# Kernel optimization log

Measured on AMD Instinct MI355X. Metric: run time of the kernel, lower is better.

The kernel has to match this reference:

```python
import jax, jax.numpy as jnp
import numpy as np

B, S, DM = 4, 2048, 512
H, D = 8, 64          # att_head, head_dim = att_dim // att_head
LEFT, RIGHT = 128, 128  # band_part(left_mask, right_mask)
LARGE = 1e30          # masked_softmax large number for fp32


def setup_inputs() -> dict:
    key = jax.random.key(0)
    ks = jax.random.split(key, 11)
    scale = 1.0 / np.sqrt(DM)
    x = jax.random.normal(ks[0], (B, S, DM), jnp.float32)
    Wq = jax.random.normal(ks[1], (DM, DM), jnp.float32) * scale
    bq = jnp.zeros((DM,), jnp.float32)
    Wk = jax.random.normal(ks[2], (DM, DM), jnp.float32) * scale
    bk = jnp.zeros((DM,), jnp.float32)
    Wv = jax.random.normal(ks[3], (DM, DM), jnp.float32) * scale
    bv = jnp.zeros((DM,), jnp.float32)
    Wo = jax.random.normal(ks[4], (DM, DM), jnp.float32) * scale
    bo = jnp.zeros((DM,), jnp.float32)
    x_len = jax.random.randint(ks[5], (B,), 0, 2048)
    return {"x": x, "Wq": Wq, "bq": bq, "Wk": Wk, "bk": bk,
            "Wv": Wv, "bv": bv, "Wo": Wo, "bo": bo, "x_len": x_len}


def reference(x, Wq, bq, Wk, bk, Wv, bv, Wo, bo, x_len):
    b, s, _ = x.shape
    # QKV projections, split into heads: [B,S,H,D]
    q = (x @ Wq + bq).reshape(b, s, H, D)
    k = (x @ Wk + bk).reshape(b, s, H, D)
    v = (x @ Wv + bv).reshape(b, s, H, D)
    # content energy: [B,H,Q,K], scaled by sqrt(head_dim)
    energy = jnp.einsum('bind,bjnd->bnij', q, k) / jnp.sqrt(jnp.float32(D))
    # banded mask (tf.linalg.band_part semantics): keep -LEFT <= j-i <= RIGHT
    i = jnp.arange(s)[:, None]
    j = jnp.arange(s)[None, :]
    band = ((j - i) <= RIGHT) & ((i - j) <= LEFT)            # [S,S]
    # key-length mask (tf.sequence_mask, expanded to [B,1,1,S])
    seq = jnp.arange(s)[None, :] < x_len[:, None]            # [B,S]
    mask = (band[None, None, :, :] & seq[:, None, None, :]).astype(energy.dtype)
    # masked softmax: energy - (1 - mask) * LARGE, softmax over keys
    att = jax.nn.softmax(energy - (1.0 - mask) * LARGE, axis=-1)
    # context: [B,Q,H,D] -> [B,S,H*D]
    ctx = jnp.einsum('bnij,bjnd->bind', att, v).reshape(b, s, H * D)
    # output projection (use_proj=True)
    return ctx @ Wo + bo
```

## Files before the change

### kernel.cpp

```cpp
#include <hip/hip_runtime.h>

#define S_LEN 2048
#define BATCH 4
#define DMODEL 512
#define NHEAD 8
#define HDIM 64
#define ROWS (BATCH * S_LEN)

using short8 = __attribute__((ext_vector_type(8))) short;
using f32x4  = __attribute__((ext_vector_type(4))) float;

__device__ __forceinline__ unsigned short f2bf(float f) {
  unsigned int u = __builtin_bit_cast(unsigned int, f);
  u += 0x7fffu + ((u >> 16) & 1u);
  return (unsigned short)(u >> 16);
}
__device__ __forceinline__ float bf2f(unsigned short h) {
  unsigned int u = ((unsigned int)h) << 16;
  return __builtin_bit_cast(float, u);
}
__device__ __forceinline__ void glds16(const void* g, void* l) {
  __builtin_amdgcn_global_load_lds((const __attribute__((address_space(1))) unsigned*)g,
                                   (__attribute__((address_space(3))) unsigned*)l, 16, 0, 0);
}

__global__ __launch_bounds__(256) void prep_kernel(const float* __restrict__ x,
                                                   const float* __restrict__ Wq,
                                                   const float* __restrict__ Wk,
                                                   const float* __restrict__ Wv,
                                                   const float* __restrict__ Wo,
                                                   unsigned short* __restrict__ xb,
                                                   unsigned short* __restrict__ WqkT,
                                                   unsigned short* __restrict__ WvT,
                                                   unsigned short* __restrict__ WoT) {
  __shared__ float t[32][33];
  const int blk = blockIdx.x, tid = threadIdx.x;
  if (blk < 2048) {
    const int base = (blk * 256 + tid) * 8;
    float4 f0 = *(const float4*)(x + base);
    float4 f1 = *(const float4*)(x + base + 4);
    uint4 o;
    o.x = (unsigned)f2bf(f0.x) | ((unsigned)f2bf(f0.y) << 16);
    o.y = (unsigned)f2bf(f0.z) | ((unsigned)f2bf(f0.w) << 16);
    o.z = (unsigned)f2bf(f1.x) | ((unsigned)f2bf(f1.y) << 16);
    o.w = (unsigned)f2bf(f1.z) | ((unsigned)f2bf(f1.w) << 16);
    *(uint4*)(xb + base) = o;
    return;
  }
  const int tb = blk - 2048;
  const int which = tb >> 8;
  const int tile = tb & 255;
  const float* W = which == 0 ? Wq : which == 1 ? Wk : which == 2 ? Wv : Wo;
  unsigned short* WT = which == 0 ? WqkT : which == 1 ? (WqkT + 512 * 512)
                      : which == 2 ? WvT : WoT;
  const int tx = tid & 31, ty = tid >> 5;
  const int x0 = (tile & 15) * 32, y0 = (tile >> 4) * 32;
#pragma unroll
  for (int r = 0; r < 4; r++)
    t[ty + 8 * r][tx] = W[(size_t)(y0 + ty + 8 * r) * DMODEL + x0 + tx];
  __syncthreads();
#pragma unroll
  for (int r = 0; r < 4; r++)
    WT[(size_t)(x0 + ty + 8 * r) * DMODEL + y0 + tx] = f2bf(t[tx][ty + 8 * r]);
}

__global__ __launch_bounds__(256, 2) void gemm_qkv_kernel(const unsigned short* __restrict__ xb,
                                                          const unsigned short* __restrict__ WqkT,
                                                          const unsigned short* __restrict__ WvT,
                                                          const float* __restrict__ bq,
                                                          const float* __restrict__ bk,
                                                          const float* __restrict__ bv,
                                                          const int* __restrict__ x_len,
                                                          unsigned short* __restrict__ Qb,
                                                          unsigned short* __restrict__ Kb,
                                                          unsigned short* __restrict__ Vt) {
  constexpr int K = DMODEL;
  __shared__ __align__(16) char smem[16384];
  char* As = smem;
  char* Bs = smem + 8192;
  const int bid = blockIdx.x;
  const bool vmode = bid < 256;
  const unsigned short *A, *Bt;
  int m0, n0;
  if (vmode) {
    m0 = (bid & 3) * 128;
    n0 = (bid >> 2) * 128;
    A = WvT; Bt = xb;
  } else {
    const int q = bid - 256;
    m0 = (q >> 3) * 128;
    n0 = (q & 7) * 128;
    A = xb; Bt = WqkT;
    const int xl = x_len[m0 >> 11];
    const int s0 = m0 & 2047;
    if (n0 >= DMODEL) { if (s0 >= xl) return; }
    else if (s0 >= xl + 128) return;
  }
  const int tid = threadIdx.x;
  const int wave = tid >> 6, lane = tid & 63;
  const int wr = wave >> 1, wc = wave & 1;
  const int lm = lane & 15, lq = lane >> 4;
  const int lr = lane >> 2;
  const int lc = (lane & 3) ^ ((lane >> 3) & 3);
  const unsigned short* gA0 = A + (size_t)(m0 + wave * 16 + lr) * K + lc * 8;
  const unsigned short* gA1 = A + (size_t)(m0 + (wave + 4) * 16 + lr) * K + lc * 8;
  const unsigned short* gB0 = Bt + (size_t)(n0 + wave * 16 + lr) * K + lc * 8;
  const unsigned short* gB1 = Bt + (size_t)(n0 + (wave + 4) * 16 + lr) * K + lc * 8;
  char* lA0 = As + wave * 1024 + lane * 16;
  char* lA1 = As + (wave + 4) * 1024 + lane * 16;
  char* lB0 = Bs + wave * 1024 + lane * 16;
  char* lB1 = Bs + (wave + 4) * 1024 + lane * 16;
  const int sw = (lm >> 1) & 3;
  int aoff[4], boff[4];
#pragma unroll
  for (int mi = 0; mi < 4; mi++)
    aoff[mi] = (wr * 64 + mi * 16 + lm) * 64 + (lq ^ sw) * 16;
#pragma unroll
  for (int ni = 0; ni < 4; ni++)
    boff[ni] = (wc * 64 + ni * 16 + lm) * 64 + (lq ^ sw) * 16;

  f32x4 acc[4][4] = {};
  for (int k0 = 0; k0 < K; k0 += 32) {
    __syncthreads();
    glds16(gA0 + k0, lA0);
    glds16(gA1 + k0, lA1);
    glds16(gB0 + k0, lB0);
    glds16(gB1 + k0, lB1);
    __syncthreads();
    short8 af[4], bfr[4];
#pragma unroll
    for (int mi = 0; mi < 4; mi++) af[mi] = *(const short8*)(As + aoff[mi]);
#pragma unroll
    for (int ni = 0; ni < 4; ni++) bfr[ni] = *(const short8*)(Bs + boff[ni]);
#pragma unroll
    for (int mi = 0; mi < 4; mi++)
#pragma unroll
      for (int ni = 0; ni < 4; ni++)
        acc[mi][ni] = __builtin_amdgcn_mfma_f32_16x16x32_bf16(af[mi], bfr[ni], acc[mi][ni], 0, 0, 0);
  }
#pragma unroll
  for (int mi = 0; mi < 4; mi++) {
    const int row0 = m0 + wr * 64 + mi * 16 + lq * 4;
#pragma unroll
    for (int ni = 0; ni < 4; ni++) {
      const int col = n0 + wc * 64 + ni * 16 + lm;
#pragma unroll
      for (int r = 0; r < 4; r++) {
        const int row = row0 + r;
        const float v = acc[mi][ni][r];
        if (vmode) {
          Vt[(size_t)row * ROWS + col] = f2bf(v + bv[row]);
        } else if (col < DMODEL) {
          Qb[(size_t)row * DMODEL + col] = f2bf(v + bq[col]);
        } else {
          Kb[(size_t)row * DMODEL + (col - DMODEL)] = f2bf(v + bk[col - DMODEL]);
        }
      }
    }
  }
}

__global__ __launch_bounds__(256, 2) void gemm_out_kernel(const unsigned short* __restrict__ A,
                                                          const unsigned short* __restrict__ Bt,
                                                          const float* __restrict__ bias,
                                                          float* __restrict__ out) {
  constexpr int K = DMODEL;
  __shared__ __align__(16) char smem[16384];
  char* As = smem;
  char* Bs = smem + 8192;
  const int tid = threadIdx.x;
  const int wave = tid >> 6, lane = tid & 63;
  const int wr = wave >> 1, wc = wave & 1;
  const int lm = lane & 15, lq = lane >> 4;
  const int m0 = blockIdx.y * 128, n0 = blockIdx.x * 128;
  const int lr = lane >> 2;
  const int lc = (lane & 3) ^ ((lane >> 3) & 3);
  const unsigned short* gA0 = A + (size_t)(m0 + wave * 16 + lr) * K + lc * 8;
  const unsigned short* gA1 = A + (size_t)(m0 + (wave + 4) * 16 + lr) * K + lc * 8;
  const unsigned short* gB0 = Bt + (size_t)(n0 + wave * 16 + lr) * K + lc * 8;
  const unsigned short* gB1 = Bt + (size_t)(n0 + (wave + 4) * 16 + lr) * K + lc * 8;
  char* lA0 = As + wave * 1024 + lane * 16;
  char* lA1 = As + (wave + 4) * 1024 + lane * 16;
  char* lB0 = Bs + wave * 1024 + lane * 16;
  char* lB1 = Bs + (wave + 4) * 1024 + lane * 16;
  const int sw = (lm >> 1) & 3;
  int aoff[4], boff[4];
#pragma unroll
  for (int mi = 0; mi < 4; mi++)
    aoff[mi] = (wr * 64 + mi * 16 + lm) * 64 + (lq ^ sw) * 16;
#pragma unroll
  for (int ni = 0; ni < 4; ni++)
    boff[ni] = (wc * 64 + ni * 16 + lm) * 64 + (lq ^ sw) * 16;

  f32x4 acc[4][4] = {};
  for (int k0 = 0; k0 < K; k0 += 32) {
    __syncthreads();
    glds16(gA0 + k0, lA0);
    glds16(gA1 + k0, lA1);
    glds16(gB0 + k0, lB0);
    glds16(gB1 + k0, lB1);
    __syncthreads();
    short8 af[4], bfr[4];
#pragma unroll
    for (int mi = 0; mi < 4; mi++) af[mi] = *(const short8*)(As + aoff[mi]);
#pragma unroll
    for (int ni = 0; ni < 4; ni++) bfr[ni] = *(const short8*)(Bs + boff[ni]);
#pragma unroll
    for (int mi = 0; mi < 4; mi++)
#pragma unroll
      for (int ni = 0; ni < 4; ni++)
        acc[mi][ni] = __builtin_amdgcn_mfma_f32_16x16x32_bf16(af[mi], bfr[ni], acc[mi][ni], 0, 0, 0);
  }
#pragma unroll
  for (int mi = 0; mi < 4; mi++) {
    const int row0 = m0 + wr * 64 + mi * 16 + lq * 4;
#pragma unroll
    for (int ni = 0; ni < 4; ni++) {
      const int col = n0 + wc * 64 + ni * 16 + lm;
#pragma unroll
      for (int r = 0; r < 4; r++)
        out[(size_t)(row0 + r) * DMODEL + col] = acc[mi][ni][r] + bias[col];
    }
  }
}

__global__ __launch_bounds__(256) void vsum_kernel(const unsigned short* __restrict__ Vt,
                                                   float* __restrict__ vs) {
  const int wid = blockIdx.x * 4 + (threadIdx.x >> 6);
  const int lane = threadIdx.x & 63;
  const int b = wid >> 9, n = wid & 511;
  const unsigned short* row = Vt + (size_t)n * ROWS + b * S_LEN;
  float s = 0.f;
#pragma unroll
  for (int it = 0; it < 4; it++) {
    uint4 v = *(const uint4*)(row + it * 512 + lane * 8);
    unsigned int w[4] = {v.x, v.y, v.z, v.w};
#pragma unroll
    for (int e = 0; e < 4; e++) {
      s += bf2f((unsigned short)(w[e] & 0xffffu));
      s += bf2f((unsigned short)(w[e] >> 16));
    }
  }
#pragma unroll
  for (int off = 1; off < 64; off <<= 1) s += __shfl_xor(s, off, 64);
  if (lane == 0) vs[(size_t)b * DMODEL + n] = s;
}

__global__ __launch_bounds__(256) void attn_kernel(const unsigned short* __restrict__ Q,
                                                   const unsigned short* __restrict__ K,
                                                   const unsigned short* __restrict__ Vt,
                                                   const int* __restrict__ x_len,
                                                   const float* __restrict__ vsum,
                                                   unsigned short* __restrict__ ctx) {
  __shared__ unsigned short Ks[32][72];
  __shared__ unsigned short Vs[64][40];
  __shared__ unsigned short Ps[4][16][40];
  const int tid = threadIdx.x;
  const int wave = tid >> 6, lane = tid & 63;
  const int lm = lane & 15, lq = lane >> 4;
  const int b = blockIdx.z, h = blockIdx.y;
  const int i0 = blockIdx.x * 64;
  const int q0 = i0 + wave * 16;
  const int xlen = x_len[b];

  const size_t qoff = (size_t)(b * S_LEN + q0 + lm) * DMODEL + h * HDIM + lq * 8;
  const short8 aq0 = *(const short8*)(Q + qoff);
  const short8 aq1 = *(const short8*)(Q + qoff + 32);

  const int krow = tid >> 3, kchk = (tid & 7) * 8;
  const int vdim = tid >> 2, vchk = (tid & 3) * 8;

  f32x4 oacc[4] = {};
  float lrow[4] = {0.f, 0.f, 0.f, 0.f};

  for (int kt = 0; kt < 10; kt++) {
    const int jt0 = i0 - 128 + kt * 32;
    if (jt0 + 31 < 0 || jt0 >= xlen) continue;
    __syncthreads();
    {
      const int jr = jt0 + krow;
      const int jrc = min(max(jr, 0), S_LEN - 1);
      *(uint4*)&Ks[krow][kchk] =
          *(const uint4*)(K + (size_t)(b * S_LEN + jrc) * DMODEL + h * HDIM + kchk);
      const int jv = jt0 + vchk;
      const int jvc = min(max(jv, 0), S_LEN - 8);
      *(uint4*)&Vs[vdim][vchk] =
          *(const uint4*)(Vt + (size_t)(h * HDIM + vdim) * ROWS + b * S_LEN + jvc);
    }
    __syncthreads();
    if (jt0 + 31 < q0 - 128 || jt0 > q0 + 143) continue;

    f32x4 sv[2];
#pragma unroll
    for (int sub = 0; sub < 2; sub++) {
      const short8 bk0 = *(const short8*)&Ks[sub * 16 + lm][lq * 8];
      const short8 bk1 = *(const short8*)&Ks[sub * 16 + lm][32 + lq * 8];
      f32x4 s = {};
      s = __builtin_amdgcn_mfma_f32_16x16x32_bf16(aq0, bk0, s, 0, 0, 0);
      s = __builtin_amdgcn_mfma_f32_16x16x32_bf16(aq1, bk1, s, 0, 0, 0);
      sv[sub] = s;
    }
    float p[2][4];
#pragma unroll
    for (int sub = 0; sub < 2; sub++) {
      const int j = jt0 + sub * 16 + lm;
      const bool jv = (j >= 0) && (j < xlen);
#pragma unroll
      for (int r = 0; r < 4; r++) {
        const int i = q0 + lq * 4 + r;
        const bool ok = jv && (j - i <= 128) && (i - j <= 128);
        const float pv = ok ? __expf(sv[sub][r] * 0.125f) : 0.f;
        p[sub][r] = pv;
        lrow[r] += pv;
      }
    }
#pragma unroll
    for (int r = 0; r < 4; r++) {
      Ps[wave][lq * 4 + r][lm] = f2bf(p[0][r]);
      Ps[wave][lq * 4 + r][16 + lm] = f2bf(p[1][r]);
    }
    const short8 pf = *(const short8*)&Ps[wave][lm][lq * 8];
#pragma unroll
    for (int dt = 0; dt < 4; dt++) {
      const short8 bv = *(const short8*)&Vs[dt * 16 + lm][lq * 8];
      oacc[dt] = __builtin_amdgcn_mfma_f32_16x16x32_bf16(pf, bv, oacc[dt], 0, 0, 0);
    }
  }
#pragma unroll
  for (int r = 0; r < 4; r++)
#pragma unroll
    for (int off = 1; off < 16; off <<= 1) lrow[r] += __shfl_xor(lrow[r], off, 64);

#pragma unroll
  for (int r = 0; r < 4; r++) {
    const int i = q0 + lq * 4 + r;
    const size_t obase = (size_t)(b * S_LEN + i) * DMODEL + h * HDIM;
    if (lrow[r] > 0.f) {
      const float inv = 1.f / lrow[r];
#pragma unroll
      for (int dt = 0; dt < 4; dt++)
        ctx[obase + dt * 16 + lm] = f2bf(oacc[dt][r] * inv);
    } else {
#pragma unroll
      for (int dt = 0; dt < 4; dt++)
        ctx[obase + dt * 16 + lm] =
            f2bf(vsum[(size_t)b * DMODEL + h * HDIM + dt * 16 + lm] * (1.f / 2048.f));
    }
  }
}

extern "C" void kernel_launch(void* const* d_in, const int* in_sizes, int n_in,
                              void* d_out, int out_size, void* d_ws, size_t ws_size,
                              hipStream_t stream) {
  (void)in_sizes; (void)n_in; (void)out_size; (void)ws_size;
  const float* x  = (const float*)d_in[0];
  const float* Wq = (const float*)d_in[1];
  const float* bq = (const float*)d_in[2];
  const float* Wk = (const float*)d_in[3];
  const float* bk = (const float*)d_in[4];
  const float* Wv = (const float*)d_in[5];
  const float* bv = (const float*)d_in[6];
  const float* Wo = (const float*)d_in[7];
  const float* bo = (const float*)d_in[8];
  const int* x_len = (const int*)d_in[9];

  char* ws = (char*)d_ws;
  const size_t MB = 1024 * 1024;
  unsigned short* xb   = (unsigned short*)(ws + 0 * MB);
  unsigned short* Qb   = (unsigned short*)(ws + 8 * MB);
  unsigned short* Kb   = (unsigned short*)(ws + 16 * MB);
  unsigned short* Vt   = (unsigned short*)(ws + 24 * MB);
  unsigned short* Cx   = (unsigned short*)(ws + 32 * MB);
  unsigned short* WqkT = (unsigned short*)(ws + 40 * MB);
  unsigned short* WvT  = (unsigned short*)(ws + 41 * MB);
  unsigned short* WoT  = (unsigned short*)(ws + 41 * MB + 512 * 1024);
  float* vsum          = (float*)(ws + 42 * MB);

  prep_kernel<<<3072, 256, 0, stream>>>(x, Wq, Wk, Wv, Wo, xb, WqkT, WvT, WoT);
  gemm_qkv_kernel<<<768, 256, 0, stream>>>(xb, WqkT, WvT, bq, bk, bv, x_len, Qb, Kb, Vt);
  vsum_kernel<<<512, 256, 0, stream>>>(Vt, vsum);
  attn_kernel<<<dim3(32, 8, 4), 256, 0, stream>>>(Qb, Kb, Vt, x_len, vsum, Cx);
  gemm_out_kernel<<<dim3(4, 64), 256, 0, stream>>>(Cx, WoT, bo, (float*)d_out);
}
```

Baseline: 149.3 us.

## Skip output GEMM for fully masked rows and use swizzled LDS loads in attention

Output-GEMM blocks whose rows all lie past x_len+128 now exit early. A new tail kernel writes those rows directly as the constant projection of the mean of V (vsum/2048 @ Wo + bo), which is what uniform softmax over fully masked rows gives. The attention kernel also switches its K/V tile loads to global_load_lds with an XOR-swizzled unpadded LDS layout, removing the register round-trip and padding. The tail kernel adds a naive per-block 512x512 matvec, which is redundant across blocks but small.

New measurement: 168.3 us. 12.7% more time.

```diff
diff --git a/kernel.cpp b/kernel.cpp
--- a/kernel.cpp
+++ b/kernel.cpp
@@ -163,16 +163,21 @@
 __global__ __launch_bounds__(256, 2) void gemm_out_kernel(const unsigned short* __restrict__ A,
                                                           const unsigned short* __restrict__ Bt,
                                                           const float* __restrict__ bias,
+                                                          const int* __restrict__ x_len,
                                                           float* __restrict__ out) {
   constexpr int K = DMODEL;
   __shared__ __align__(16) char smem[16384];
   char* As = smem;
   char* Bs = smem + 8192;
+  const int m0 = blockIdx.y * 128, n0 = blockIdx.x * 128;
+  {
+    const int xl = x_len[m0 >> 11];
+    if ((m0 & 2047) >= min(S_LEN, xl + 128)) return;
+  }
   const int tid = threadIdx.x;
   const int wave = tid >> 6, lane = tid & 63;
   const int wr = wave >> 1, wc = wave & 1;
   const int lm = lane & 15, lq = lane >> 4;
-  const int m0 = blockIdx.y * 128, n0 = blockIdx.x * 128;
   const int lr = lane >> 2;
   const int lc = (lane & 3) ^ ((lane >> 3) & 3);
   const unsigned short* gA0 = A + (size_t)(m0 + wave * 16 + lr) * K + lc * 8;
@@ -224,6 +229,30 @@
   }
 }
 
+__global__ __launch_bounds__(256) void tail_kernel(const float* __restrict__ vsum,
+                                                   const unsigned short* __restrict__ WoT,
+                                                   const float* __restrict__ bo,
+                                                   const int* __restrict__ x_len,
+                                                   float* __restrict__ out) {
+  const int b = blockIdx.y, j = blockIdx.x;
+  const int t0 = min(S_LEN, x_len[b] + 128);
+  const int r0 = j * 128, r1 = r0 + 128;
+  if (r1 <= t0) return;
+  __shared__ float tv[512];
+  const float* vs = vsum + b * DMODEL;
+  for (int c = threadIdx.x; c < DMODEL; c += 256) {
+    const unsigned short* wrow = WoT + (size_t)c * DMODEL;
+    float acc = 0.f;
+    for (int k = 0; k < DMODEL; k++) acc += vs[k] * bf2f(wrow[k]);
+    tv[c] = bo[c] + acc * (1.f / 2048.f);
+  }
+  __syncthreads();
+  const int rs = max(r0, t0);
+  const float4 val = ((const float4*)tv)[threadIdx.x & 127];
+  for (int r = rs + (threadIdx.x >> 7); r < r1; r += 2)
+    ((float4*)(out + (size_t)(b * S_LEN + r) * DMODEL))[threadIdx.x & 127] = val;
+}
+
 __global__ __launch_bounds__(256) void vsum_kernel(const unsigned short* __restrict__ Vt,
                                                    float* __restrict__ vs) {
   const int wid = blockIdx.x * 4 + (threadIdx.x >> 6);
@@ -252,8 +281,8 @@
                                                    const int* __restrict__ x_len,
                                                    const float* __restrict__ vsum,
                                                    unsigned short* __restrict__ ctx) {
-  __shared__ unsigned short Ks[32][72];
-  __shared__ unsigned short Vs[64][40];
+  __shared__ __align__(16) unsigned short Ks[32 * 64];
+  __shared__ __align__(16) unsigned short Vs[64 * 32];
   __shared__ unsigned short Ps[4][16][40];
   const int tid = threadIdx.x;
   const int wave = tid >> 6, lane = tid & 63;
@@ -267,8 +296,13 @@
   const short8 aq0 = *(const short8*)(Q + qoff);
   const short8 aq1 = *(const short8*)(Q + qoff + 32);
 
-  const int krow = tid >> 3, kchk = (tid & 7) * 8;
-  const int vdim = tid >> 2, vchk = (tid & 3) * 8;
+  const int kr = lane >> 3, kp = lane & 7, klc = kp ^ kr;
+  unsigned short* dstK = Ks + wave * 512 + lane * 8;
+  const int vr = lane >> 2, vp = lane & 3;
+  const int vrow = wave * 16 + vr;
+  const int vlc = vp ^ ((vr >> 1) & 3);
+  unsigned short* dstV = Vs + wave * 512 + lane * 8;
+  const int swk = lm & 7, swv = (lm >> 1) & 3;
 
   f32x4 oacc[4] = {};
   float lrow[4] = {0.f, 0.f, 0.f, 0.f};
@@ -278,14 +312,12 @@
     if (jt0 + 31 < 0 || jt0 >= xlen) continue;
     __syncthreads();
     {
-      const int jr = jt0 + krow;
-      const int jrc = min(max(jr, 0), S_LEN - 1);
-      *(uint4*)&Ks[krow][kchk] =
-          *(const uint4*)(K + (size_t)(b * S_LEN + jrc) * DMODEL + h * HDIM + kchk);
-      const int jv = jt0 + vchk;
+      const int krow_g = jt0 + wave * 8 + kr;
+      const int krc = min(max(krow_g, 0), S_LEN - 1);
+      glds16(K + (size_t)(b * S_LEN + krc) * DMODEL + h * HDIM + klc * 8, dstK);
+      const int jv = jt0 + vlc * 8;
       const int jvc = min(max(jv, 0), S_LEN - 8);
-      *(uint4*)&Vs[vdim][vchk] =
-          *(const uint4*)(Vt + (size_t)(h * HDIM + vdim) * ROWS + b * S_LEN + jvc);
+      glds16(Vt + (size_t)(h * HDIM + vrow) * ROWS + b * S_LEN + jvc, dstV);
     }
     __syncthreads();
     if (jt0 + 31 < q0 - 128 || jt0 > q0 + 143) continue;
@@ -293,8 +325,9 @@
     f32x4 sv[2];
 #pragma unroll
     for (int sub = 0; sub < 2; sub++) {
-      const short8 bk0 = *(const short8*)&Ks[sub * 16 + lm][lq * 8];
-      const short8 bk1 = *(const short8*)&Ks[sub * 16 + lm][32 + lq * 8];
+      const int krow = (sub * 16 + lm) * 64;
+      const short8 bk0 = *(const short8*)&Ks[krow + ((lq ^ swk) * 8)];
+      const short8 bk1 = *(const short8*)&Ks[krow + (((lq + 4) ^ swk) * 8)];
       f32x4 s = {};
       s = __builtin_amdgcn_mfma_f32_16x16x32_bf16(aq0, bk0, s, 0, 0, 0);
       s = __builtin_amdgcn_mfma_f32_16x16x32_bf16(aq1, bk1, s, 0, 0, 0);
@@ -322,7 +355,7 @@
     const short8 pf = *(const short8*)&Ps[wave][lm][lq * 8];
 #pragma unroll
     for (int dt = 0; dt < 4; dt++) {
-      const short8 bv = *(const short8*)&Vs[dt * 16 + lm][lq * 8];
+      const short8 bv = *(const short8*)&Vs[(dt * 16 + lm) * 32 + ((lq ^ swv) * 8)];
       oacc[dt] = __builtin_amdgcn_mfma_f32_16x16x32_bf16(pf, bv, oacc[dt], 0, 0, 0);
     }
   }
@@ -380,5 +413,6 @@
   gemm_qkv_kernel<<<768, 256, 0, stream>>>(xb, WqkT, WvT, bq, bk, bv, x_len, Qb, Kb, Vt);
   vsum_kernel<<<512, 256, 0, stream>>>(Vt, vsum);
   attn_kernel<<<dim3(32, 8, 4), 256, 0, stream>>>(Qb, Kb, Vt, x_len, vsum, Cx);
-  gemm_out_kernel<<<dim3(4, 64), 256, 0, stream>>>(Cx, WoT, bo, (float*)d_out);
-}
+  gemm_out_kernel<<<dim3(4, 64), 256, 0, stream>>>(Cx, WoT, bo, x_len, (float*)d_out);
+  tail_kernel<<<dim3(16, 4), 256, 0, stream>>>(vsum, WoT, bo, x_len, (float*)d_out);
+}
```

## Skip fully-masked query tiles; precompute shared output row for masked tail

Applied to the files above, without the earlier changes.

Query rows beyond x_len+128 have no valid keys, so their output is a constant row per batch: mean(V) projected through Wo plus bias. A small tailrow kernel computes this row once per batch. The attention kernel now exits early for those tiles, and the output GEMM fills those blocks by broadcasting the row instead of running the MFMA loop. This avoids attention and projection work on rows that are fully masked, at the cost of one extra small launch and a result that depends on the runtime x_len distribution.

Result: no change. 148.9 us (-0.2%).

```diff
diff --git a/kernel.cpp b/kernel.cpp
--- a/kernel.cpp
+++ b/kernel.cpp
@@ -160,70 +160,6 @@
   }
 }
 
-__global__ __launch_bounds__(256, 2) void gemm_out_kernel(const unsigned short* __restrict__ A,
-                                                          const unsigned short* __restrict__ Bt,
-                                                          const float* __restrict__ bias,
-                                                          float* __restrict__ out) {
-  constexpr int K = DMODEL;
-  __shared__ __align__(16) char smem[16384];
-  char* As = smem;
-  char* Bs = smem + 8192;
-  const int tid = threadIdx.x;
-  const int wave = tid >> 6, lane = tid & 63;
-  const int wr = wave >> 1, wc = wave & 1;
-  const int lm = lane & 15, lq = lane >> 4;
-  const int m0 = blockIdx.y * 128, n0 = blockIdx.x * 128;
-  const int lr = lane >> 2;
-  const int lc = (lane & 3) ^ ((lane >> 3) & 3);
-  const unsigned short* gA0 = A + (size_t)(m0 + wave * 16 + lr) * K + lc * 8;
-  const unsigned short* gA1 = A + (size_t)(m0 + (wave + 4) * 16 + lr) * K + lc * 8;
-  const unsigned short* gB0 = Bt + (size_t)(n0 + wave * 16 + lr) * K + lc * 8;
-  const unsigned short* gB1 = Bt + (size_t)(n0 + (wave + 4) * 16 + lr) * K + lc * 8;
-  char* lA0 = As + wave * 1024 + lane * 16;
-  char* lA1 = As + (wave + 4) * 1024 + lane * 16;
-  char* lB0 = Bs + wave * 1024 + lane * 16;
-  char* lB1 = Bs + (wave + 4) * 1024 + lane * 16;
-  const int sw = (lm >> 1) & 3;
-  int aoff[4], boff[4];
-#pragma unroll
-  for (int mi = 0; mi < 4; mi++)
-    aoff[mi] = (wr * 64 + mi * 16 + lm) * 64 + (lq ^ sw) * 16;
-#pragma unroll
-  for (int ni = 0; ni < 4; ni++)
-    boff[ni] = (wc * 64 + ni * 16 + lm) * 64 + (lq ^ sw) * 16;
-
-  f32x4 acc[4][4] = {};
-  for (int k0 = 0; k0 < K; k0 += 32) {
-    __syncthreads();
-    glds16(gA0 + k0, lA0);
-    glds16(gA1 + k0, lA1);
-    glds16(gB0 + k0, lB0);
-    glds16(gB1 + k0, lB1);
-    __syncthreads();
-    short8 af[4], bfr[4];
-#pragma unroll
-    for (int mi = 0; mi < 4; mi++) af[mi] = *(const short8*)(As + aoff[mi]);
-#pragma unroll
-    for (int ni = 0; ni < 4; ni++) bfr[ni] = *(const short8*)(Bs + boff[ni]);
-#pragma unroll
-    for (int mi = 0; mi < 4; mi++)
-#pragma unroll
-      for (int ni = 0; ni < 4; ni++)
-        acc[mi][ni] = __builtin_amdgcn_mfma_f32_16x16x32_bf16(af[mi], bfr[ni], acc[mi][ni], 0, 0, 0);
-  }
-#pragma unroll
-  for (int mi = 0; mi < 4; mi++) {
-    const int row0 = m0 + wr * 64 + mi * 16 + lq * 4;
-#pragma unroll
-    for (int ni = 0; ni < 4; ni++) {
-      const int col = n0 + wc * 64 + ni * 16 + lm;
-#pragma unroll
-      for (int r = 0; r < 4; r++)
-        out[(size_t)(row0 + r) * DMODEL + col] = acc[mi][ni][r] + bias[col];
-    }
-  }
-}
-
 __global__ __launch_bounds__(256) void vsum_kernel(const unsigned short* __restrict__ Vt,
                                                    float* __restrict__ vs) {
   const int wid = blockIdx.x * 4 + (threadIdx.x >> 6);
@@ -244,6 +180,33 @@
 #pragma unroll
   for (int off = 1; off < 64; off <<= 1) s += __shfl_xor(s, off, 64);
   if (lane == 0) vs[(size_t)b * DMODEL + n] = s;
+}
+
+__global__ __launch_bounds__(256) void tailrow_kernel(const float* __restrict__ vsum,
+                                                      const unsigned short* __restrict__ WoT,
+                                                      const float* __restrict__ bo,
+                                                      float* __restrict__ trow) {
+  const int b = blockIdx.y;
+  const int wave = threadIdx.x >> 6, lane = threadIdx.x & 63;
+  const float* vs = vsum + b * DMODEL + lane * 8;
+  float vreg[8];
+  *(float4*)vreg = *(const float4*)vs;
+  *(float4*)(vreg + 4) = *(const float4*)(vs + 4);
+#pragma unroll
+  for (int ci = 0; ci < 8; ci++) {
+    const int c = blockIdx.x * 32 + wave * 8 + ci;
+    const uint4 wv = *(const uint4*)(WoT + (size_t)c * DMODEL + lane * 8);
+    const unsigned int w[4] = {wv.x, wv.y, wv.z, wv.w};
+    float acc = 0.f;
+#pragma unroll
+    for (int e = 0; e < 4; e++) {
+      acc += vreg[2 * e] * bf2f((unsigned short)(w[e] & 0xffffu));
+      acc += vreg[2 * e + 1] * bf2f((unsigned short)(w[e] >> 16));
+    }
+#pragma unroll
+    for (int off = 1; off < 64; off <<= 1) acc += __shfl_xor(acc, off, 64);
+    if (lane == 0) trow[b * DMODEL + c] = bo[c] + acc * (1.f / 2048.f);
+  }
 }
 
 __global__ __launch_bounds__(256) void attn_kernel(const unsigned short* __restrict__ Q,
@@ -262,6 +225,8 @@
   const int i0 = blockIdx.x * 64;
   const int q0 = i0 + wave * 16;
   const int xlen = x_len[b];
+  const int t0 = min(S_LEN, xlen + 128);
+  if ((i0 & ~127) >= t0) return;
 
   const size_t qoff = (size_t)(b * S_LEN + q0 + lm) * DMODEL + h * HDIM + lq * 8;
   const short8 aq0 = *(const short8*)(Q + qoff);
@@ -345,6 +310,83 @@
       for (int dt = 0; dt < 4; dt++)
         ctx[obase + dt * 16 + lm] =
             f2bf(vsum[(size_t)b * DMODEL + h * HDIM + dt * 16 + lm] * (1.f / 2048.f));
+    }
+  }
+}
+
+__global__ __launch_bounds__(256, 2) void gemm_out_kernel(const unsigned short* __restrict__ A,
+                                                          const unsigned short* __restrict__ Bt,
+                                                          const float* __restrict__ bias,
+                                                          const int* __restrict__ x_len,
+                                                          const float* __restrict__ trow,
+                                                          float* __restrict__ out) {
+  constexpr int K = DMODEL;
+  __shared__ __align__(16) char smem[16384];
+  char* As = smem;
+  char* Bs = smem + 8192;
+  const int tid = threadIdx.x;
+  const int m0 = blockIdx.y * 128, n0 = blockIdx.x * 128;
+  {
+    const int xl = x_len[m0 >> 11];
+    if ((m0 & 2047) >= min(S_LEN, xl + 128)) {
+      const float4 val = *(const float4*)(trow + (m0 >> 11) * DMODEL + n0 + (tid & 31) * 4);
+      float* obase = out + (size_t)m0 * DMODEL + n0 + (tid & 31) * 4;
+#pragma unroll
+      for (int r = tid >> 5; r < 128; r += 8)
+        *(float4*)(obase + (size_t)r * DMODEL) = val;
+      return;
+    }
+  }
+  const int wave = tid >> 6, lane = tid & 63;
+  const int wr = wave >> 1, wc = wave & 1;
+  const int lm = lane & 15, lq = lane >> 4;
+  const int lr = lane >> 2;
+  const int lc = (lane & 3) ^ ((lane >> 3) & 3);
+  const unsigned short* gA0 = A + (size_t)(m0 + wave * 16 + lr) * K + lc * 8;
+  const unsigned short* gA1 = A + (size_t)(m0 + (wave + 4) * 16 + lr) * K + lc * 8;
+  const unsigned short* gB0 = Bt + (size_t)(n0 + wave * 16 + lr) * K + lc * 8;
+  const unsigned short* gB1 = Bt + (size_t)(n0 + (wave + 4) * 16 + lr) * K + lc * 8;
+  char* lA0 = As + wave * 1024 + lane * 16;
+  char* lA1 = As + (wave + 4) * 1024 + lane * 16;
+  char* lB0 = Bs + wave * 1024 + lane * 16;
+  char* lB1 = Bs + (wave + 4) * 1024 + lane * 16;
+  const int sw = (lm >> 1) & 3;
+  int aoff[4], boff[4];
+#pragma unroll
+  for (int mi = 0; mi < 4; mi++)
+    aoff[mi] = (wr * 64 + mi * 16 + lm) * 64 + (lq ^ sw) * 16;
+#pragma unroll
+  for (int ni = 0; ni < 4; ni++)
+    boff[ni] = (wc * 64 + ni * 16 + lm) * 64 + (lq ^ sw) * 16;
+
+  f32x4 acc[4][4] = {};
+  for (int k0 = 0; k0 < K; k0 += 32) {
+    __syncthreads();
+    glds16(gA0 + k0, lA0);
+    glds16(gA1 + k0, lA1);
+    glds16(gB0 + k0, lB0);
+    glds16(gB1 + k0, lB1);
+    __syncthreads();
+    short8 af[4], bfr[4];
+#pragma unroll
+    for (int mi = 0; mi < 4; mi++) af[mi] = *(const short8*)(As + aoff[mi]);
+#pragma unroll
+    for (int ni = 0; ni < 4; ni++) bfr[ni] = *(const short8*)(Bs + boff[ni]);
+#pragma unroll
+    for (int mi = 0; mi < 4; mi++)
+#pragma unroll
+      for (int ni = 0; ni < 4; ni++)
+        acc[mi][ni] = __builtin_amdgcn_mfma_f32_16x16x32_bf16(af[mi], bfr[ni], acc[mi][ni], 0, 0, 0);
+  }
+#pragma unroll
+  for (int mi = 0; mi < 4; mi++) {
+    const int row0 = m0 + wr * 64 + mi * 16 + lq * 4;
+#pragma unroll
+    for (int ni = 0; ni < 4; ni++) {
+      const int col = n0 + wc * 64 + ni * 16 + lm;
+#pragma unroll
+      for (int r = 0; r < 4; r++)
+        out[(size_t)(row0 + r) * DMODEL + col] = acc[mi][ni][r] + bias[col];
     }
   }
 }
@@ -375,10 +417,12 @@
   unsigned short* WvT  = (unsigned short*)(ws + 41 * MB);
   unsigned short* WoT  = (unsigned short*)(ws + 41 * MB + 512 * 1024);
   float* vsum          = (float*)(ws + 42 * MB);
+  float* trow          = (float*)(ws + 42 * MB + 8192);
 
   prep_kernel<<<3072, 256, 0, stream>>>(x, Wq, Wk, Wv, Wo, xb, WqkT, WvT, WoT);
   gemm_qkv_kernel<<<768, 256, 0, stream>>>(xb, WqkT, WvT, bq, bk, bv, x_len, Qb, Kb, Vt);
   vsum_kernel<<<512, 256, 0, stream>>>(Vt, vsum);
+  tailrow_kernel<<<dim3(16, 4), 256, 0, stream>>>(vsum, WoT, bo, trow);
   attn_kernel<<<dim3(32, 8, 4), 256, 0, stream>>>(Qb, Kb, Vt, x_len, vsum, Cx);
-  gemm_out_kernel<<<dim3(4, 64), 256, 0, stream>>>(Cx, WoT, bo, (float*)d_out);
-}
+  gemm_out_kernel<<<dim3(4, 64), 256, 0, stream>>>(Cx, WoT, bo, x_len, trow, (float*)d_out);
+}
```
